# Performance work log

Hardware: AMD Instinct MI355X
Metric: run time of the kernel (lower is better)

The kernel has to match this reference:

```python
import jax, jax.numpy as jnp
import numpy as np

B, S, H = 2, 2048, 4096
NH, NKV, HD = 32, 8, 128
RD = 64  # partial rotary dim = head_dim * partial_rotary_factor
THETA = 10000.0


def setup_inputs() -> dict:
    key = jax.random.key(0)
    ks = jax.random.split(key, 6)
    hidden_states = jax.random.normal(ks[0], (B, S, H), dtype=jnp.float32)
    wq = jax.random.normal(ks[1], (H, NH * HD), dtype=jnp.float32) * 0.02
    wk = jax.random.normal(ks[2], (H, NKV * HD), dtype=jnp.float32) * 0.02
    wv = jax.random.normal(ks[3], (H, NKV * HD), dtype=jnp.float32) * 0.02
    wo = jax.random.normal(ks[4], (NH * HD, H), dtype=jnp.float32) * 0.02
    # default RoPE over rotary_dim=RD: inv_freq has RD//2 entries, emb = cat(freqs, freqs)
    inv_freq = 1.0 / (THETA ** (jnp.arange(0, RD, 2, dtype=jnp.float32) / RD))  # [RD//2]
    pos = jnp.arange(S, dtype=jnp.float32)
    freqs = pos[:, None] * inv_freq[None, :]               # [S, RD//2]
    emb = jnp.concatenate([freqs, freqs], axis=-1)          # [S, RD]
    cos = jnp.broadcast_to(jnp.cos(emb)[None], (B, S, RD))
    sin = jnp.broadcast_to(jnp.sin(emb)[None], (B, S, RD))
    return {"hidden_states": hidden_states, "wq": wq, "wk": wk, "wv": wv, "wo": wo,
            "cos": cos, "sin": sin}


def _rotate_half_interleaved(x):
    # GLM-style interleaved rotate: pairs (x0,x1) -> (-x1,x0)
    x1 = x[..., 0::2]
    x2 = x[..., 1::2]
    return jnp.stack((-x2, x1), axis=-1).reshape(x.shape)


def _apply_partial_rope(x, cos_i, sin_i):
    x_rot, x_pass = x[..., :RD], x[..., RD:]
    x_rot = x_rot * cos_i + _rotate_half_interleaved(x_rot) * sin_i
    return jnp.concatenate([x_rot, x_pass], axis=-1)


def reference(hidden_states, wq, wk, wv, wo, cos, sin):
    b, s, _ = hidden_states.shape
    # projections -> [B, nheads, S, head_dim]
    q = (hidden_states @ wq).reshape(b, s, NH, HD).transpose(0, 2, 1, 3)
    k = (hidden_states @ wk).reshape(b, s, NKV, HD).transpose(0, 2, 1, 3)
    v = (hidden_states @ wv).reshape(b, s, NKV, HD).transpose(0, 2, 1, 3)
    # GLM partial rotary: take first half of cos/sin and repeat-interleave by 2
    cos_i = jnp.repeat(cos[..., : RD // 2], 2, axis=-1)[:, None]  # [B,1,S,RD]
    sin_i = jnp.repeat(sin[..., : RD // 2], 2, axis=-1)[:, None]
    q = _apply_partial_rope(q, cos_i, sin_i)
    k = _apply_partial_rope(k, cos_i, sin_i)
    # repeat_kv for GQA
    rep = NH // NKV
    k = jnp.repeat(k, rep, axis=1)
    v = jnp.repeat(v, rep, axis=1)
    # causal SDPA, scaling = head_dim**-0.5
    scores = jnp.einsum('bhqd,bhkd->bhqk', q, k) * (HD ** -0.5)
    causal = jnp.tril(jnp.ones((s, s), dtype=bool))
    scores = jnp.where(causal[None, None], scores, jnp.finfo(scores.dtype).min)
    probs = jax.nn.softmax(scores, axis=-1)
    out = jnp.einsum('bhqk,bhkd->bhqd', probs, v)
    out = out.transpose(0, 2, 1, 3).reshape(b, s, NH * HD)
    return out @ wo
```

## Files before the change

kernel.cpp:

```cpp
#include <hip/hip_runtime.h>


typedef _Float16 f16;
typedef _Float16 f16x8 __attribute__((ext_vector_type(8)));
typedef float f32x4 __attribute__((ext_vector_type(4)));
typedef float f32x16 __attribute__((ext_vector_type(16)));

static constexpr int Bn = 2, Sn = 2048, Hn = 4096, NH = 32, NKV = 8, HD = 128;
static constexpr float QSC = 0.08838834764831845f * 1.44269504088896340736f;

#define AS1 __attribute__((address_space(1)))
#define AS3 __attribute__((address_space(3)))

__device__ __forceinline__ void async_ld16(const void* g, void* l) {
    __builtin_amdgcn_global_load_lds((const AS1 void*)g, (AS3 void*)l, 16, 0, 0);
}

__device__ __forceinline__ unsigned pk2(float a, float b) {
    unsigned r;
    asm("v_cvt_pkrtz_f16_f32 %0, %1, %2" : "=v"(r) : "v"(a), "v"(b));
    return r;
}

__device__ __forceinline__ float fexp2(float x) {
    float r;
    asm("v_exp_f32 %0, %1" : "=v"(r) : "v"(x));
    return r;
}

__global__ __launch_bounds__(256) void k_prep(
    const float* __restrict__ hs, f16* __restrict__ hid,
    const float* __restrict__ wq, const float* __restrict__ wk,
    const float* __restrict__ wv, const float* __restrict__ wo,
    f16* __restrict__ wqkv_t, f16* __restrict__ wo_t) {
    int bid = blockIdx.x;
    if (bid < 8192) {
        long i = ((long)bid * 256 + threadIdx.x) * 8;
        float4 a = *(const float4*)(hs + i);
        float4 b = *(const float4*)(hs + i + 4);
        f16x8 o = {(f16)a.x, (f16)a.y, (f16)a.z, (f16)a.w,
                   (f16)b.x, (f16)b.y, (f16)b.z, (f16)b.w};
        *(f16x8*)(hid + i) = o;
        return;
    }
    bid -= 8192;
    const float* src;
    f16* dst;
    int N, bx, by;
    if (bid < 4096)      { src = wq; dst = wqkv_t;                    N = 4096; bx = bid & 63; by = bid >> 6; }
    else if (bid < 5120) { bid -= 4096; src = wk; dst = wqkv_t + (long)4096 * 4096; N = 1024; bx = bid & 15; by = bid >> 4; }
    else if (bid < 6144) { bid -= 5120; src = wv; dst = wqkv_t + (long)5120 * 4096; N = 1024; bx = bid & 15; by = bid >> 4; }
    else                 { bid -= 6144; src = wo; dst = wo_t;         N = 4096; bx = bid & 63; by = bid >> 6; }
    __shared__ float tile[64][65];
    const int k0 = by * 64, n0 = bx * 64;
    const int tx = threadIdx.x & 63, ty = threadIdx.x >> 6;
#pragma unroll
    for (int r = ty; r < 64; r += 4)
        tile[r][tx] = src[(long)(k0 + r) * N + (n0 + tx)];
    __syncthreads();
#pragma unroll
    for (int r = ty; r < 64; r += 4)
        dst[(long)(n0 + r) * 4096 + (k0 + tx)] = (f16)tile[tx][r];
}

__device__ __forceinline__ void gemm384_core(
    const f16* __restrict__ A, const f16* __restrict__ Bt,
    char* L, int m0, int n0, f32x4 acc[8][6]) {
    const int t = threadIdx.x, lane = t & 63, wave = t >> 6;
    const int wm = wave >> 2, wn = wave & 3;
    const int fr = lane & 15, fg = lane >> 4;

    const int srowL = wave * 8 + (lane >> 3);
    const int scol  = 8 * ((lane & 7) ^ (lane >> 3));
    const f16* ga = A  + (long)(m0 + srowL) * 4096 + scol;
    const f16* gb = Bt + (long)(n0 + srowL) * 4096 + scol;
    const int woff = wave * 1024;

    auto ST = [&](int sel, int c, int row0, int kt) {
        const f16* g = sel ? gb : ga;
        async_ld16(g + (long)row0 * 4096 + kt * 64,
                   L + c * 81920 + sel * 32768 + row0 * 128 + woff);
    };

    ST(0, 0, 0, 0); ST(0, 0, 64, 0); ST(0, 0, 128, 0); ST(0, 0, 192, 0);
#pragma unroll
    for (int r = 0; r < 384; r += 64) ST(1, 0, r, 0);
#pragma unroll
    for (int r = 0; r < 384; r += 64) ST(1, 1, r, 1);
    ST(0, 1, 0, 1); ST(0, 1, 128, 1);
    asm volatile("s_waitcnt vmcnt(8)" ::: "memory");
    __builtin_amdgcn_s_barrier();

    const int abase = wm * 128;
    const int bbase = wn * 96;

    for (int tt = 0; tt < 64; ++tt) {
        const int c = tt & 1;
        const char* bufA = L + c * 81920;
        const char* bufB = bufA + 32768;
        f16x8 bf[6];

#pragma unroll
        for (int ph = 0; ph < 4; ++ph) {
            const int ks = ph >> 1, mh = ph & 1;
            if (mh == 0) {
#pragma unroll
                for (int nf = 0; nf < 6; ++nf) {
                    int r = bbase + nf * 16 + fr;
                    bf[nf] = *(const f16x8*)(bufB + r * 128 +
                                 ((ks * 64 + 16 * fg) ^ ((r & 7) << 4)));
                }
            }
            f16x8 af[4];
#pragma unroll
            for (int i = 0; i < 4; ++i) {
                int r = abase + mh * 64 + i * 16 + fr;
                af[i] = *(const f16x8*)(bufA + r * 128 +
                             ((ks * 64 + 16 * fg) ^ ((r & 7) << 4)));
            }
            if (ph == 0) { if (tt + 1 < 64) { ST(0, c ^ 1,  64, tt + 1);
                                              ST(0, c ^ 1, 192, tt + 1); } }
            if (ph == 3) { if (tt + 2 < 64) {
#pragma unroll
                for (int r = 0; r < 384; r += 64) ST(1, c, r, tt + 2);
                ST(0, c, 0, tt + 2); ST(0, c, 128, tt + 2); } }
            __builtin_amdgcn_s_barrier();
            __builtin_amdgcn_s_setprio(1);
#pragma unroll
            for (int i = 0; i < 4; ++i)
#pragma unroll
                for (int nf = 0; nf < 6; ++nf)
                    acc[mh * 4 + i][nf] = __builtin_amdgcn_mfma_f32_16x16x32_f16(
                        af[i], bf[nf], acc[mh * 4 + i][nf], 0, 0, 0);
            __builtin_amdgcn_s_setprio(0);
            if (ph == 3) {
                if (tt < 62)       asm volatile("s_waitcnt vmcnt(8)" ::: "memory");
                else if (tt == 62) asm volatile("s_waitcnt vmcnt(0)" ::: "memory");
            }
            __builtin_amdgcn_s_barrier();
        }
    }
}

__device__ __forceinline__ void gemm256_core(
    const f16* __restrict__ A, const f16* __restrict__ Bt,
    char* L, int m0, int n0, f32x4 acc[8][4]) {
    const int t = threadIdx.x, lane = t & 63, wave = t >> 6;
    const int wm = wave >> 2, wn = wave & 3;
    const int fr = lane & 15, fg = lane >> 4;

    const int srowL = wave * 8 + (lane >> 3);
    const int scol  = 8 * ((lane & 7) ^ (lane >> 3));
    const f16* ga = A  + (long)(m0 + srowL) * 4096 + scol;
    const f16* gb = Bt + (long)(n0 + srowL) * 4096 + scol;
    const int woff = wave * 1024;

    auto ST = [&](int sel, int c, int row0, int kt) {
        const f16* g = sel ? gb : ga;
        async_ld16(g + (long)row0 * 4096 + kt * 64,
                   L + c * 65536 + sel * 32768 + row0 * 128 + woff);
    };

    ST(0, 0, 0, 0);   ST(0, 0, 64, 0);  ST(0, 0, 128, 0); ST(0, 0, 192, 0);
    ST(1, 0, 0, 0);   ST(1, 0, 64, 0);  ST(1, 0, 128, 0); ST(1, 0, 192, 0);
    ST(1, 1, 0, 1);   ST(1, 1, 64, 1);  ST(1, 1, 128, 1); ST(1, 1, 192, 1);
    ST(0, 1, 0, 1);   ST(0, 1, 128, 1);
    asm volatile("s_waitcnt vmcnt(6)" ::: "memory");
    __builtin_amdgcn_s_barrier();

    const int abase = wm * 128;
    const int bbase = wn * 64;

    for (int tt = 0; tt < 64; ++tt) {
        const int c = tt & 1;
        const char* bufA = L + c * 65536;
        const char* bufB = bufA + 32768;
        f16x8 bf[2][4];

#pragma unroll
        for (int q = 0; q < 4; ++q) {
            if (q == 0) {
#pragma unroll
                for (int ks = 0; ks < 2; ++ks)
#pragma unroll
                    for (int nf = 0; nf < 4; ++nf) {
                        int r = bbase + nf * 16 + fr;
                        bf[ks][nf] = *(const f16x8*)(bufB + r * 128 +
                                        ((ks * 64 + 16 * fg) ^ ((r & 7) << 4)));
                    }
            }
            f16x8 af[2][2];
#pragma unroll
            for (int ks = 0; ks < 2; ++ks)
#pragma unroll
                for (int i = 0; i < 2; ++i) {
                    int r = abase + (2 * q + i) * 16 + fr;
                    af[ks][i] = *(const f16x8*)(bufA + r * 128 +
                                    ((ks * 64 + 16 * fg) ^ ((r & 7) << 4)));
                }
            if (q == 0) { if (tt + 1 < 64) { ST(0, c ^ 1,  64, tt + 1);
                                             ST(0, c ^ 1, 192, tt + 1); } }
            if (q == 1) { if (tt + 2 < 64) { ST(1, c,   0, tt + 2);
                                             ST(1, c,  64, tt + 2); } }
            if (q == 2) { if (tt + 2 < 64) { ST(1, c, 128, tt + 2);
                                             ST(1, c, 192, tt + 2); } }
            if (q == 3) { if (tt + 2 < 64) { ST(0, c,   0, tt + 2);
                                             ST(0, c, 128, tt + 2); } }
            __builtin_amdgcn_s_barrier();
            __builtin_amdgcn_s_setprio(1);
#pragma unroll
            for (int ks = 0; ks < 2; ++ks)
#pragma unroll
                for (int i = 0; i < 2; ++i)
#pragma unroll
                    for (int nf = 0; nf < 4; ++nf)
                        acc[2 * q + i][nf] = __builtin_amdgcn_mfma_f32_16x16x32_f16(
                            af[ks][i], bf[ks][nf], acc[2 * q + i][nf], 0, 0, 0);
            __builtin_amdgcn_s_setprio(0);
            if (q == 3) {
                if (tt < 62)       asm volatile("s_waitcnt vmcnt(6)" ::: "memory");
                else if (tt == 62) asm volatile("s_waitcnt vmcnt(0)" ::: "memory");
            }
            __builtin_amdgcn_s_barrier();
        }
    }
}

__global__ __launch_bounds__(512) void k_gemm_qkv(
    const f16* __restrict__ A, const f16* __restrict__ Bt,
    f16* __restrict__ q, f16* __restrict__ kk_, f16* __restrict__ vt,
    const float* __restrict__ cosb, const float* __restrict__ sinb) {
    __shared__ __align__(16) char L[163840];
    const int bid = blockIdx.x;
    const int swzb = (bid & 7) * 32 + (bid >> 3);
    const int m0 = (swzb >> 4) * 256, n0 = (swzb & 15) * 384;
    f32x4 acc[8][6] = {};
    gemm384_core(A, Bt, L, m0, n0, acc);

    const int lane = threadIdx.x & 63, wave = threadIdx.x >> 6;
    const int wm = wave >> 2, wn = wave & 3;
    const int fr = lane & 15, fg = lane >> 4;
#pragma unroll
    for (int mf = 0; mf < 8; ++mf) {
        int r0 = m0 + wm * 128 + mf * 16 + 4 * fg;
        int b = r0 >> 11, s = r0 & (Sn - 1);
        const float* cb_ = cosb + ((long)b * Sn + s) * 64;
        const float* sb_ = sinb + ((long)b * Sn + s) * 64;
#pragma unroll
        for (int nf = 0; nf < 6; ++nf) {
            int cc = n0 + wn * 96 + nf * 16 + fr;
            int d = cc & 127;
            if (cc < 5120) {
                float vals[4];
#pragma unroll
                for (int e = 0; e < 4; ++e) vals[e] = acc[mf][nf][e];
                if (d < 64) {
                    int ci = d >> 1;
                    bool odd = (d & 1);
#pragma unroll
                    for (int e = 0; e < 4; ++e) {
                        float p = __shfl_xor(vals[e], 1, 64);
                        float c = cb_[e * 64 + ci], sv = sb_[e * 64 + ci];
                        vals[e] = odd ? (vals[e] * c + p * sv)
                                      : (vals[e] * c - p * sv);
                    }
                }
                if (cc < 4096) {
                    int h = cc >> 7;
#pragma unroll
                    for (int e = 0; e < 4; ++e)
                        q[(((long)b * NH + h) * Sn + s + e) * HD + d] =
                            (f16)(vals[e] * QSC);
                } else {
                    int h = (cc - 4096) >> 7;
#pragma unroll
                    for (int e = 0; e < 4; ++e)
                        kk_[(((long)b * NKV + h) * Sn + s + e) * HD + d] =
                            (f16)vals[e];
                }
            } else {
                int h = (cc - 5120) >> 7;
                uint2 w = {pk2(acc[mf][nf][0], acc[mf][nf][1]),
                           pk2(acc[mf][nf][2], acc[mf][nf][3])};
                *(uint2*)&vt[(((long)b * NKV + h) * HD + d) * Sn + s] = w;
            }
        }
    }
}

__global__ __launch_bounds__(512) void k_gemm_out(
    const f16* __restrict__ A, const f16* __restrict__ Bt,
    float* __restrict__ out) {
    __shared__ __align__(16) char L[131072];
    const int bid = blockIdx.x;
    const int swzb = (bid & 7) * 32 + (bid >> 3);
    const int m0 = (swzb >> 4) * 256, n0 = (swzb & 15) * 256;
    f32x4 acc[8][4] = {};
    gemm256_core(A, Bt, L, m0, n0, acc);

    const int lane = threadIdx.x & 63, wave = threadIdx.x >> 6;
    const int wm = wave >> 2, wn = wave & 3;
    const int fr = lane & 15, fg = lane >> 4;
#pragma unroll
    for (int mf = 0; mf < 8; ++mf) {
        int r0 = m0 + wm * 128 + mf * 16 + 4 * fg;
#pragma unroll
        for (int nf = 0; nf < 4; ++nf) {
            int cc = n0 + wn * 64 + nf * 16 + fr;
#pragma unroll
            for (int e = 0; e < 4; ++e)
                out[(long)(r0 + e) * 4096 + cc] = acc[mf][nf][e];
        }
    }
}


__device__ __forceinline__ f16x8 ld_sw256(const f16* base, int r, int c) {
    int byte = r * 256 + ((c * 2) ^ ((r & 7) << 4));
    return *(const f16x8*)((const char*)base + byte);
}
__device__ __forceinline__ f16x8 ld_sw128(const f16* base, int r, int c) {
    int byte = r * 128 + ((c * 2) ^ ((r & 7) << 4));
    return *(const f16x8*)((const char*)base + byte);
}

__device__ __forceinline__ void stage_k(const f16* __restrict__ Kb, f16* ksm,
                                        int k0, int wave, int lane) {
#pragma unroll
    for (int i = 0; i < 2; ++i) {
        int dbase = (i * 8 + wave) * 1024;
        int d = dbase + lane * 16;
        int row = d >> 8;
        int cb = (d & 255) ^ ((row & 7) << 4);
        async_ld16(Kb + (long)(k0 + row) * HD + (cb >> 1), (char*)ksm + dbase);
    }
}
__device__ __forceinline__ void stage_v(const f16* __restrict__ Vb, f16* vsm,
                                        int k0, int wave, int lane) {
#pragma unroll
    for (int i = 0; i < 2; ++i) {
        int dbase = (i * 8 + wave) * 1024;
        int d = dbase + lane * 16;
        int row = d >> 7;
        int cb = (d & 127) ^ ((row & 7) << 4);
        async_ld16(Vb + (long)row * Sn + k0 + (cb >> 1), (char*)vsm + dbase);
    }
}

__global__ __launch_bounds__(512) void k_attn(
    const f16* __restrict__ Q, const f16* __restrict__ K,
    const f16* __restrict__ Vt, f16* __restrict__ O) {
    __shared__ __align__(16) f16 Ksm[2][64 * 128];
    __shared__ __align__(16) f16 Vsm[2][128 * 64];

    const int id = blockIdx.x;
    const int kvh = id & 7;
    const int r_ = id >> 3;
    const int pos = r_ & 7;
    const int qt = (pos & 1) ? (pos >> 1) : (7 - (pos >> 1));
    const int hg = (r_ >> 3) & 3;
    const int b  = r_ >> 5;
    const int h  = kvh * 4 + hg;
    const int q0 = qt * 256;
    const int t = threadIdx.x, lane = t & 63, wave = t >> 6;
    const int q0w = q0 + wave * 32;
    const int lq = lane & 31, hi = lane >> 5;

    const f16* Qb = Q + ((long)(b * NH + h) * Sn) * HD;
    const f16* Kb = K + ((long)(b * NKV + kvh) * Sn) * HD;
    const f16* Vb = Vt + ((long)(b * NKV + kvh) * HD) * Sn;

    f16x8 qf[8];
#pragma unroll
    for (int s = 0; s < 8; ++s)
        qf[s] = *(const f16x8*)&Qb[(long)(q0w + lq) * HD + 16 * s + 8 * hi];

    f32x16 oacc[4] = {};
    float mrun = -1e30f, lrun = 0.f;

    const int nt = q0 / 64 + 4;
    stage_k(Kb, Ksm[0], 0, wave, lane);
    stage_v(Vb, Vsm[0], 0, wave, lane);

    for (int kt = 0; kt < nt; ++kt) {
        const int k0 = kt * 64;
        const int cur = kt & 1;
        if (kt + 1 < nt) {
            stage_k(Kb, Ksm[cur ^ 1], (kt + 1) * 64, wave, lane);
            stage_v(Vb, Vsm[cur ^ 1], (kt + 1) * 64, wave, lane);
            asm volatile("s_waitcnt vmcnt(4)" ::: "memory");
        } else {
            asm volatile("s_waitcnt vmcnt(0)" ::: "memory");
        }
        __builtin_amdgcn_s_barrier();

        if (k0 <= q0w + 31) {
            f32x16 st[2] = {};
#pragma unroll
            for (int s = 0; s < 8; ++s) {
                f16x8 kf0 = ld_sw256(Ksm[cur], lq,      16 * s + 8 * hi);
                f16x8 kf1 = ld_sw256(Ksm[cur], 32 + lq, 16 * s + 8 * hi);
                st[0] = __builtin_amdgcn_mfma_f32_32x32x16_f16(kf0, qf[s], st[0], 0, 0, 0);
                st[1] = __builtin_amdgcn_mfma_f32_32x32x16_f16(kf1, qf[s], st[1], 0, 0, 0);
            }
            const bool full = (k0 + 63 <= q0w);
            if (!full) {
#pragma unroll
                for (int mt = 0; mt < 2; ++mt)
#pragma unroll
                    for (int r = 0; r < 16; ++r) {
                        int kvv = k0 + 32 * mt + (r & 3) + 8 * (r >> 2) + 4 * hi;
                        if (kvv > q0w + lq) st[mt][r] = -1e30f;
                    }
            }
            float pm = st[0][0];
#pragma unroll
            for (int r = 1; r < 16; ++r) pm = fmaxf(pm, st[0][r]);
#pragma unroll
            for (int r = 0; r < 16; ++r) pm = fmaxf(pm, st[1][r]);
            pm = fmaxf(pm, __shfl_xor(pm, 32, 64));
            if (__any(pm > mrun + 8.f)) {
                float mn = fmaxf(mrun, pm);
                float sc = fexp2(mrun - mn);
                mrun = mn;
                lrun *= sc;
                float scr[16];
#pragma unroll
                for (int r = 0; r < 16; ++r)
                    scr[r] = __shfl(sc, (r & 3) + 8 * (r >> 2) + 4 * hi, 64);
#pragma unroll
                for (int db = 0; db < 4; ++db)
#pragma unroll
                    for (int r = 0; r < 16; ++r)
                        oacc[db][r] *= scr[r];
            }
            unsigned pw[2][8];
#pragma unroll
            for (int mt = 0; mt < 2; ++mt)
#pragma unroll
                for (int i = 0; i < 8; ++i) {
                    float p0 = fexp2(st[mt][2 * i]     - mrun);
                    float p1 = fexp2(st[mt][2 * i + 1] - mrun);
                    lrun += p0 + p1;
                    pw[mt][i] = pk2(p0, p1);
                }
#pragma unroll
            for (int s = 0; s < 4; ++s) {
                const int mt = s >> 1, sl = s & 1;
                unsigned a0 = pw[mt][4 * sl], a1 = pw[mt][4 * sl + 1];
                unsigned a2 = pw[mt][4 * sl + 2], a3 = pw[mt][4 * sl + 3];
                unsigned own0 = hi ? a2 : a0, own1 = hi ? a3 : a1;
                unsigned snd0 = hi ? a0 : a2, snd1 = hi ? a1 : a3;
                unsigned rx0 = (unsigned)__shfl_xor((int)snd0, 32, 64);
                unsigned rx1 = (unsigned)__shfl_xor((int)snd1, 32, 64);
                union { unsigned u[4]; f16x8 v; } pu;
                pu.u[0] = hi ? rx0 : own0;
                pu.u[1] = hi ? rx1 : own1;
                pu.u[2] = hi ? own0 : rx0;
                pu.u[3] = hi ? own1 : rx1;
#pragma unroll
                for (int db = 0; db < 4; ++db) {
                    f16x8 vf = ld_sw128(Vsm[cur], 32 * db + lq, 16 * s + 8 * hi);
                    oacc[db] = __builtin_amdgcn_mfma_f32_32x32x16_f16(pu.v, vf, oacc[db], 0, 0, 0);
                }
            }
        }
        __builtin_amdgcn_s_barrier();
    }

    lrun += __shfl_xor(lrun, 32, 64);
    float li = 1.f / lrun;
    float ir[16];
#pragma unroll
    for (int r = 0; r < 16; ++r)
        ir[r] = __shfl(li, (r & 3) + 8 * (r >> 2) + 4 * hi, 64);
#pragma unroll
    for (int db = 0; db < 4; ++db)
#pragma unroll
        for (int r = 0; r < 16; ++r) {
            int qloc = (r & 3) + 8 * (r >> 2) + 4 * hi;
            long tok = (long)b * Sn + q0w + qloc;
            O[tok * (NH * HD) + h * HD + 32 * db + lq] = (f16)(oacc[db][r] * ir[r]);
        }
}

__global__ void k_ws_fail(float* out) { out[0] = 1.0e9f; }

extern "C" void kernel_launch(void* const* d_in, const int* in_sizes, int n_in,
                              void* d_out, int out_size, void* d_ws, size_t ws_size,
                              hipStream_t stream) {
    const float* hs   = (const float*)d_in[0];
    const float* wq   = (const float*)d_in[1];
    const float* wk   = (const float*)d_in[2];
    const float* wv   = (const float*)d_in[3];
    const float* wo   = (const float*)d_in[4];
    const float* cosb = (const float*)d_in[5];
    const float* sinb = (const float*)d_in[6];
    float* out = (float*)d_out;

    const size_t OFF_WQKV = 0;
    const size_t OFF_WO   = 50331648;
    const size_t OFF_HID  = 83886080;
    const size_t OFF_Q    = 117440512;
    const size_t OFF_K    = 150994944;
    const size_t OFF_VT   = 167772160;
    const size_t WS_NEED  = 176160768;
    if (ws_size < WS_NEED) { k_ws_fail<<<1, 1, 0, stream>>>(out); return; }

    char* ws = (char*)d_ws;
    f16* wqkv_t = (f16*)(ws + OFF_WQKV);
    f16* wo_t   = (f16*)(ws + OFF_WO);
    f16* hid    = (f16*)(ws + OFF_HID);
    f16* qb     = (f16*)(ws + OFF_Q);
    f16* kb     = (f16*)(ws + OFF_K);
    f16* vtb    = (f16*)(ws + OFF_VT);

    k_prep<<<dim3(18432), 256, 0, stream>>>(hs, hid, wq, wk, wv, wo, wqkv_t, wo_t);
    k_gemm_qkv<<<dim3(256), 512, 0, stream>>>(hid, wqkv_t, qb, kb, vtb, cosb, sinb);
    k_attn<<<dim3(512), 512, 0, stream>>>(qb, kb, vtb, hid);
    k_gemm_out<<<dim3(256), 512, 0, stream>>>(hid, wo_t, out);
}
```

Before: 522.2 us.

## Use 4-wave 128x128 per-wave tiles in output projection GEMM

The output projection GEMM drops from 8 waves (512 threads) to 4 waves (256 threads) per block. Each wave now computes a 128x128 sub-tile with 8x8 accumulator fragments instead of 128x64, so each LDS fragment load feeds more MFMAs. Staging loads are doubled per thread to keep the same 256x256 block tile, and the vmcnt waits and prefetch schedule are adjusted to match. This cuts LDS read traffic per FLOP, at the cost of higher register pressure (256 accumulator floats per thread), fewer waves to hide latency, and a bigger burst of prefetches in the last phase.

```diff
diff --git a/kernel.cpp b/kernel.cpp
--- a/kernel.cpp
+++ b/kernel.cpp
@@ -142,11 +142,11 @@
     }
 }
 
-__device__ __forceinline__ void gemm256_core(
+__device__ __forceinline__ void gemm2_core(
     const f16* __restrict__ A, const f16* __restrict__ Bt,
-    char* L, int m0, int n0, f32x4 acc[8][4]) {
+    char* L, int m0, int n0, f32x4 acc[8][8]) {
     const int t = threadIdx.x, lane = t & 63, wave = t >> 6;
-    const int wm = wave >> 2, wn = wave & 3;
+    const int wm = wave >> 1, wn = wave & 1;
     const int fr = lane & 15, fg = lane >> 4;
 
     const int srowL = wave * 8 + (lane >> 3);
@@ -160,65 +160,61 @@
         async_ld16(g + (long)row0 * 4096 + kt * 64,
                    L + c * 65536 + sel * 32768 + row0 * 128 + woff);
     };
-
-    ST(0, 0, 0, 0);   ST(0, 0, 64, 0);  ST(0, 0, 128, 0); ST(0, 0, 192, 0);
-    ST(1, 0, 0, 0);   ST(1, 0, 64, 0);  ST(1, 0, 128, 0); ST(1, 0, 192, 0);
-    ST(1, 1, 0, 1);   ST(1, 1, 64, 1);  ST(1, 1, 128, 1); ST(1, 1, 192, 1);
-    ST(0, 1, 0, 1);   ST(0, 1, 128, 1);
-    asm volatile("s_waitcnt vmcnt(6)" ::: "memory");
+    auto ST64 = [&](int sel, int c, int row0, int kt) {
+        ST(sel, c, row0, kt); ST(sel, c, row0 + 32, kt);
+    };
+
+    ST64(0, 0, 0, 0); ST64(0, 0, 64, 0); ST64(0, 0, 128, 0); ST64(0, 0, 192, 0);
+    ST64(1, 0, 0, 0); ST64(1, 0, 64, 0); ST64(1, 0, 128, 0); ST64(1, 0, 192, 0);
+    ST64(1, 1, 0, 1); ST64(1, 1, 64, 1); ST64(1, 1, 128, 1); ST64(1, 1, 192, 1);
+    ST64(0, 1, 0, 1); ST64(0, 1, 128, 1);
+    asm volatile("s_waitcnt vmcnt(12)" ::: "memory");
     __builtin_amdgcn_s_barrier();
 
     const int abase = wm * 128;
-    const int bbase = wn * 64;
+    const int bbase = wn * 128;
 
     for (int tt = 0; tt < 64; ++tt) {
         const int c = tt & 1;
         const char* bufA = L + c * 65536;
         const char* bufB = bufA + 32768;
-        f16x8 bf[2][4];
-
-#pragma unroll
-        for (int q = 0; q < 4; ++q) {
-            if (q == 0) {
-#pragma unroll
-                for (int ks = 0; ks < 2; ++ks)
-#pragma unroll
-                    for (int nf = 0; nf < 4; ++nf) {
-                        int r = bbase + nf * 16 + fr;
-                        bf[ks][nf] = *(const f16x8*)(bufB + r * 128 +
-                                        ((ks * 64 + 16 * fg) ^ ((r & 7) << 4)));
-                    }
-            }
-            f16x8 af[2][2];
-#pragma unroll
-            for (int ks = 0; ks < 2; ++ks)
-#pragma unroll
-                for (int i = 0; i < 2; ++i) {
-                    int r = abase + (2 * q + i) * 16 + fr;
-                    af[ks][i] = *(const f16x8*)(bufA + r * 128 +
-                                    ((ks * 64 + 16 * fg) ^ ((r & 7) << 4)));
+        f16x8 bf[8];
+
+#pragma unroll
+        for (int ph = 0; ph < 4; ++ph) {
+            const int ks = ph >> 1, mh = ph & 1;
+            if (mh == 0) {
+#pragma unroll
+                for (int nf = 0; nf < 8; ++nf) {
+                    int r = bbase + nf * 16 + fr;
+                    bf[nf] = *(const f16x8*)(bufB + r * 128 +
+                                 ((ks * 64 + 16 * fg) ^ ((r & 7) << 4)));
                 }
-            if (q == 0) { if (tt + 1 < 64) { ST(0, c ^ 1,  64, tt + 1);
-                                             ST(0, c ^ 1, 192, tt + 1); } }
-            if (q == 1) { if (tt + 2 < 64) { ST(1, c,   0, tt + 2);
-                                             ST(1, c,  64, tt + 2); } }
-            if (q == 2) { if (tt + 2 < 64) { ST(1, c, 128, tt + 2);
-                                             ST(1, c, 192, tt + 2); } }
-            if (q == 3) { if (tt + 2 < 64) { ST(0, c,   0, tt + 2);
-                                             ST(0, c, 128, tt + 2); } }
+            }
+            f16x8 af[4];
+#pragma unroll
+            for (int i = 0; i < 4; ++i) {
+                int r = abase + mh * 64 + i * 16 + fr;
+                af[i] = *(const f16x8*)(bufA + r * 128 +
+                             ((ks * 64 + 16 * fg) ^ ((r & 7) << 4)));
+            }
+            if (ph == 0) { if (tt + 1 < 64) { ST64(0, c ^ 1,  64, tt + 1);
+                                              ST64(0, c ^ 1, 192, tt + 1); } }
+            if (ph == 3) { if (tt + 2 < 64) {
+                ST64(1, c, 0, tt + 2); ST64(1, c, 64, tt + 2);
+                ST64(1, c, 128, tt + 2); ST64(1, c, 192, tt + 2);
+                ST64(0, c, 0, tt + 2); ST64(0, c, 128, tt + 2); } }
             __builtin_amdgcn_s_barrier();
             __builtin_amdgcn_s_setprio(1);
 #pragma unroll
-            for (int ks = 0; ks < 2; ++ks)
-#pragma unroll
-                for (int i = 0; i < 2; ++i)
-#pragma unroll
-                    for (int nf = 0; nf < 4; ++nf)
-                        acc[2 * q + i][nf] = __builtin_amdgcn_mfma_f32_16x16x32_f16(
-                            af[ks][i], bf[ks][nf], acc[2 * q + i][nf], 0, 0, 0);
+            for (int i = 0; i < 4; ++i)
+#pragma unroll
+                for (int nf = 0; nf < 8; ++nf)
+                    acc[mh * 4 + i][nf] = __builtin_amdgcn_mfma_f32_16x16x32_f16(
+                        af[i], bf[nf], acc[mh * 4 + i][nf], 0, 0, 0);
             __builtin_amdgcn_s_setprio(0);
-            if (q == 3) {
-                if (tt < 62)       asm volatile("s_waitcnt vmcnt(6)" ::: "memory");
+            if (ph == 3) {
+                if (tt < 62)       asm volatile("s_waitcnt vmcnt(12)" ::: "memory");
                 else if (tt == 62) asm volatile("s_waitcnt vmcnt(0)" ::: "memory");
             }
             __builtin_amdgcn_s_barrier();
@@ -288,25 +284,25 @@
     }
 }
 
-__global__ __launch_bounds__(512) void k_gemm_out(
+__global__ __launch_bounds__(256, 1) void k_gemm_out(
     const f16* __restrict__ A, const f16* __restrict__ Bt,
     float* __restrict__ out) {
     __shared__ __align__(16) char L[131072];
     const int bid = blockIdx.x;
     const int swzb = (bid & 7) * 32 + (bid >> 3);
     const int m0 = (swzb >> 4) * 256, n0 = (swzb & 15) * 256;
-    f32x4 acc[8][4] = {};
-    gemm256_core(A, Bt, L, m0, n0, acc);
+    f32x4 acc[8][8] = {};
+    gemm2_core(A, Bt, L, m0, n0, acc);
 
     const int lane = threadIdx.x & 63, wave = threadIdx.x >> 6;
-    const int wm = wave >> 2, wn = wave & 3;
+    const int wm = wave >> 1, wn = wave & 1;
     const int fr = lane & 15, fg = lane >> 4;
 #pragma unroll
     for (int mf = 0; mf < 8; ++mf) {
         int r0 = m0 + wm * 128 + mf * 16 + 4 * fg;
 #pragma unroll
-        for (int nf = 0; nf < 4; ++nf) {
-            int cc = n0 + wn * 64 + nf * 16 + fr;
+        for (int nf = 0; nf < 8; ++nf) {
+            int cc = n0 + wn * 128 + nf * 16 + fr;
 #pragma unroll
             for (int e = 0; e < 4; ++e)
                 out[(long)(r0 + e) * 4096 + cc] = acc[mf][nf][e];
@@ -518,5 +514,5 @@
     k_prep<<<dim3(18432), 256, 0, stream>>>(hs, hid, wq, wk, wv, wo, wqkv_t, wo_t);
     k_gemm_qkv<<<dim3(256), 512, 0, stream>>>(hid, wqkv_t, qb, kb, vtb, cosb, sinb);
     k_attn<<<dim3(512), 512, 0, stream>>>(qb, kb, vtb, hid);
-    k_gemm_out<<<dim3(256), 512, 0, stream>>>(hid, wo_t, out);
-}
+    k_gemm_out<<<dim3(256), 256, 0, stream>>>(hid, wo_t, out);
+}
```

Result: slower. 544.5 us (+4.3%).
